# Kernel optimization log

Hardware: AMD Instinct MI355X
Metric: run time of the kernel (lower is better)

## Reference

```python
import jax, jax.numpy as jnp
import numpy as np

N_EMBD = 1024
N_HEAD = 16


def setup_inputs() -> dict:
    key = jax.random.key(0)
    ks = jax.random.split(key, 5)
    s = 0.02
    x = jax.random.normal(ks[0], (4, 2048, N_EMBD), dtype=jnp.float32)
    W_attn = jax.random.normal(ks[1], (N_EMBD, 3 * N_EMBD), dtype=jnp.float32) * s
    b_attn = jnp.zeros((3 * N_EMBD,), dtype=jnp.float32)
    W_proj = jax.random.normal(ks[2], (N_EMBD, N_EMBD), dtype=jnp.float32) * s
    b_proj = jnp.zeros((N_EMBD,), dtype=jnp.float32)
    return {"x": x, "W_attn": W_attn, "b_attn": b_attn, "W_proj": W_proj, "b_proj": b_proj}


def reference(x, W_attn, b_attn, W_proj, b_proj):
    B, T, C = x.shape
    H = N_HEAD
    D = C // H
    qkv = x @ W_attn + b_attn  # [B,T,3C]
    q, k, v = jnp.split(qkv, 3, axis=-1)
    # [B,H,T,D]
    q = q.reshape(B, T, H, D).transpose(0, 2, 1, 3)
    k = k.reshape(B, T, H, D).transpose(0, 2, 1, 3)
    v = v.reshape(B, T, H, D).transpose(0, 2, 1, 3)
    att = jnp.einsum('bhqd,bhkd->bhqk', q, k) * (1.0 / np.sqrt(D))
    causal = jnp.tril(jnp.ones((T, T), dtype=bool))
    att = jnp.where(causal[None, None], att, -jnp.inf)
    att = jax.nn.softmax(att, axis=-1)
    y = jnp.einsum('bhqk,bhkd->bhqd', att, v)
    y = y.transpose(0, 2, 1, 3).reshape(B, T, C)
    return y @ W_proj + b_proj
```

## Files before the change

kernel.cpp:

```cpp
#include <hip/hip_runtime.h>
#include <hip/hip_bf16.h>

#define B_ 4
#define T_ 2048
#define C_ 1024
#define H_ 16
#define D_ 64
#define N3_ 3072
#define M_ (B_*T_)

typedef __bf16 bf16x8 __attribute__((ext_vector_type(8)));
typedef float f32x4 __attribute__((ext_vector_type(4)));

__device__ __forceinline__ unsigned short f2bf(float f){
  __bf16 h = (__bf16)f;
  return __builtin_bit_cast(unsigned short, h);
}
__device__ __forceinline__ unsigned int pk2(float a, float b){
  return (unsigned int)f2bf(a) | ((unsigned int)f2bf(b)<<16);
}
__device__ __forceinline__ void gload_lds16(const unsigned short* g, unsigned short* l){
  __builtin_amdgcn_global_load_lds(
      (const __attribute__((address_space(1))) void*)g,
      (__attribute__((address_space(3))) void*)l, 16, 0, 0);
}

__global__ __launch_bounds__(256) void x_cvt(
    const float* __restrict__ X, unsigned short* __restrict__ Xb)
{
  const size_t i = ((size_t)blockIdx.x*256 + threadIdx.x)*8;
  float4 f0 = *(const float4*)(X+i);
  float4 f1 = *(const float4*)(X+i+4);
  uint4 w = make_uint4(pk2(f0.x,f0.y), pk2(f0.z,f0.w), pk2(f1.x,f1.y), pk2(f1.z,f1.w));
  *(uint4*)(Xb+i) = w;
}

__global__ __launch_bounds__(256) void transpose_cvt(
    const float* __restrict__ src, unsigned short* __restrict__ dst, int K, int N)
{
  __shared__ float tile[32][33];
  const int tx = threadIdx.x & 31, ty = threadIdx.x >> 5;
  const int nt = blockIdx.x * 32, kt = blockIdx.y * 32;
  #pragma unroll
  for (int i=0;i<32;i+=8) tile[ty+i][tx] = src[(size_t)(kt+ty+i)*N + nt+tx];
  __syncthreads();
  #pragma unroll
  for (int i=0;i<32;i+=8) dst[(size_t)(nt+ty+i)*K + kt+tx] = f2bf(tile[tx][ty+i]);
}

__global__ __launch_bounds__(256) void qkv_gemm(
    const unsigned short* __restrict__ Xb, const unsigned short* __restrict__ Wt,
    const float* __restrict__ bias,
    unsigned short* __restrict__ Qb, unsigned short* __restrict__ Kb,
    unsigned short* __restrict__ Vt)
{
  __shared__ __align__(16) unsigned short As[128][32];
  __shared__ __align__(16) unsigned short Bs[128][32];
  const int tid = threadIdx.x;
  const int nbx = N3_/128;
  const int cpx = (nbx*(M_/128))/8;
  const int id0 = (int)blockIdx.x;
  const int swz = (id0 & 7)*cpx + (id0 >> 3);
  const int m0 = (swz / nbx)*128, n0 = (swz % nbx)*128;
  const int wv = tid>>6, lane = tid&63, lm = lane&15, lq = lane>>4;
  const int wr = wv>>1, wc = wv&1;
  f32x4 acc[4][4] = {};
  const int schunk = (lane&3) ^ ((lane>>3)&3);
  const unsigned short* gA = Xb + (size_t)(m0 + wv*32 + (lane>>2))*C_ + schunk*8;
  const unsigned short* gB = Wt + (size_t)(n0 + wv*32 + (lane>>2))*C_ + schunk*8;
  unsigned short* lA0 = &As[wv*32][0];
  unsigned short* lA1 = &As[wv*32+16][0];
  unsigned short* lB0 = &Bs[wv*32][0];
  unsigned short* lB1 = &Bs[wv*32+16][0];
  const int rkey = (lm>>1)&3;
  for (int k0=0;k0<C_;k0+=32){
    __syncthreads();
    gload_lds16(gA + k0,            lA0);
    gload_lds16(gA + 16*C_ + k0,    lA1);
    gload_lds16(gB + k0,            lB0);
    gload_lds16(gB + 16*C_ + k0,    lB1);
    __syncthreads();
    bf16x8 a[4], b[4];
    #pragma unroll
    for (int mt=0;mt<4;mt++) a[mt] = *(const bf16x8*)&As[wr*64+mt*16+lm][(lq^rkey)*8];
    #pragma unroll
    for (int nt=0;nt<4;nt++) b[nt] = *(const bf16x8*)&Bs[wc*64+nt*16+lm][(lq^rkey)*8];
    #pragma unroll
    for (int mt=0;mt<4;mt++)
      #pragma unroll
      for (int nt=0;nt<4;nt++)
        acc[mt][nt] = __builtin_amdgcn_mfma_f32_16x16x32_bf16(a[mt], b[nt], acc[mt][nt], 0,0,0);
  }
  const int sel = n0>>10;
  const float qsc = (sel==0) ? 0.18033688f : 1.0f;
  #pragma unroll
  for (int mt=0;mt<4;mt++){
    const int grow = m0 + wr*64 + mt*16 + lq*4;
    const int bb = grow>>11, tt0 = grow&2047;
    #pragma unroll
    for (int nt=0;nt<4;nt++){
      const int gcol = n0 + wc*64 + nt*16 + lm;
      const int hh = (gcol>>6)&15, dd = gcol&63;
      const float bv = bias[gcol];
      if (sel==2){
        ushort4 pv;
        pv.x = f2bf(acc[mt][nt][0] + bv);
        pv.y = f2bf(acc[mt][nt][1] + bv);
        pv.z = f2bf(acc[mt][nt][2] + bv);
        pv.w = f2bf(acc[mt][nt][3] + bv);
        *(ushort4*)&Vt[ ((size_t)(bb*H_+hh)*D_ + dd)*T_ + tt0 ] = pv;
      } else {
        unsigned short* dst = (sel==0) ? Qb : Kb;
        #pragma unroll
        for (int r=0;r<4;r++)
          dst[ ((size_t)(bb*H_+hh)*T_ + tt0 + r)*D_ + dd ] = f2bf((acc[mt][nt][r] + bv)*qsc);
      }
    }
  }
}

__global__ __launch_bounds__(256, 4) void flash_attn(
    const unsigned short* __restrict__ Qb, const unsigned short* __restrict__ Kb,
    const unsigned short* __restrict__ Vt, unsigned short* __restrict__ Yb)
{
  __shared__ __align__(16) unsigned short Ks[2][64][64];
  __shared__ __align__(16) unsigned short Vs[2][64][64];
  __shared__ __align__(16) unsigned short Ps[64][64];
  const int tid = threadIdx.x;
  const int wv = tid>>6, lane = tid&63, lm = lane&15, lq = lane>>4;
  const int id = (int)blockIdx.x;
  const int bh = id & 63;
  const int qi = 31 - (id >> 6);
  const int qbase = qi*64;
  const unsigned short* Qh = Qb + (size_t)bh*T_*D_;
  const unsigned short* Kh = Kb + (size_t)bh*T_*D_;
  const unsigned short* Vh = Vt + (size_t)bh*D_*T_;
  bf16x8 aq[2];
  {
    const int q = qbase + wv*16 + lm;
    aq[0] = *(const bf16x8*)&Qh[(size_t)q*D_ + lq*8];
    aq[1] = *(const bf16x8*)&Qh[(size_t)q*D_ + 32 + lq*8];
  }
  f32x4 o[4] = {};
  float l_r[4] = {0.f,0.f,0.f,0.f};
  const int srl = lane>>3;
  const int sc  = (lane&7) ^ srl;
  const unsigned short* kg = Kh + (size_t)(wv*16 + srl)*D_ + sc*8;
  const unsigned short* vg = Vh + (size_t)(wv*16 + srl)*T_ + sc*8;
  const int keyR = lm&7;
  {
    unsigned short* lk = &Ks[0][wv*16][0];
    unsigned short* lv = &Vs[0][wv*16][0];
    gload_lds16(kg,            lk);
    gload_lds16(kg + 8*D_,     lk + 8*64);
    gload_lds16(vg,            lv);
    gload_lds16(vg + 8*T_,     lv + 8*64);
  }
  for (int j=0;j<=qi;j++){
    const int cb = j&1;
    __syncthreads();
    if (j < qi){
      unsigned short* lk = &Ks[cb^1][wv*16][0];
      unsigned short* lv = &Vs[cb^1][wv*16][0];
      gload_lds16(kg + (size_t)((j+1)*64  )*D_, lk);
      gload_lds16(kg + (size_t)((j+1)*64+8)*D_, lk + 8*64);
      gload_lds16(vg + (j+1)*64,                lv);
      gload_lds16(vg + 8*T_ + (j+1)*64,         lv + 8*64);
    }
    f32x4 s[4] = {};
    __builtin_amdgcn_s_setprio(1);
    #pragma unroll
    for (int nt=0;nt<4;nt++){
      bf16x8 bk0 = *(const bf16x8*)&Ks[cb][nt*16+lm][((lq  )^keyR)*8];
      bf16x8 bk1 = *(const bf16x8*)&Ks[cb][nt*16+lm][((lq+4)^keyR)*8];
      s[nt] = __builtin_amdgcn_mfma_f32_16x16x32_bf16(aq[0], bk0, s[nt], 0,0,0);
      s[nt] = __builtin_amdgcn_mfma_f32_16x16x32_bf16(aq[1], bk1, s[nt], 0,0,0);
    }
    __builtin_amdgcn_s_setprio(0);
    if (j==qi){
      const int qrow0 = wv*16 + lq*4;
      #pragma unroll
      for (int nt=0;nt<4;nt++){
        const int col = nt*16+lm;
        #pragma unroll
        for (int r=0;r<4;r++)
          s[nt][r] = (col <= qrow0+r) ? exp2f(s[nt][r]) : 0.f;
      }
    } else {
      #pragma unroll
      for (int nt=0;nt<4;nt++)
        #pragma unroll
        for (int r=0;r<4;r++)
          s[nt][r] = exp2f(s[nt][r]);
    }
    #pragma unroll
    for (int r=0;r<4;r++)
      l_r[r] += (s[0][r]+s[1][r]) + (s[2][r]+s[3][r]);
    #pragma unroll
    for (int nt=0;nt<4;nt++)
      #pragma unroll
      for (int r=0;r<4;r++){
        const int row = wv*16 + lq*4 + r;
        const int ch  = (2*nt + (lm>>3)) ^ (row&7);
        Ps[row][ch*8 + (lm&7)] = f2bf(s[nt][r]);
      }
    __builtin_amdgcn_s_setprio(1);
    #pragma unroll
    for (int kc=0;kc<2;kc++){
      bf16x8 ap = *(const bf16x8*)&Ps[wv*16+lm][((kc*4+lq)^keyR)*8];
      #pragma unroll
      for (int dt=0;dt<4;dt++){
        bf16x8 bv = *(const bf16x8*)&Vs[cb][dt*16+lm][((kc*4+lq)^keyR)*8];
        o[dt] = __builtin_amdgcn_mfma_f32_16x16x32_bf16(bv, ap, o[dt], 0,0,0);
      }
    }
    __builtin_amdgcn_s_setprio(0);
  }
  #pragma unroll
  for (int r=0;r<4;r++){
    float rs = l_r[r];
    rs += __shfl_xor(rs,1); rs += __shfl_xor(rs,2);
    rs += __shfl_xor(rs,4); rs += __shfl_xor(rs,8);
    l_r[r] = rs;
  }
  const int srcl = (lm>>2)<<4;
  float lv0v = __shfl(l_r[0], srcl);
  float lv1v = __shfl(l_r[1], srcl);
  float lv2v = __shfl(l_r[2], srcl);
  float lv3v = __shfl(l_r[3], srcl);
  const int rr = lm&3;
  float linv = (rr==0) ? lv0v : (rr==1) ? lv1v : (rr==2) ? lv2v : lv3v;
  linv = 1.0f/linv;
  const int bb = bh>>4, hh = bh&15;
  const int q = qbase + wv*16 + lm;
  #pragma unroll
  for (int dt=0;dt<4;dt++){
    ushort4 y;
    y.x = f2bf(o[dt][0]*linv);
    y.y = f2bf(o[dt][1]*linv);
    y.z = f2bf(o[dt][2]*linv);
    y.w = f2bf(o[dt][3]*linv);
    *(ushort4*)&Yb[ ((size_t)bb*T_ + q)*C_ + hh*64 + dt*16 + lq*4 ] = y;
  }
}

__global__ __launch_bounds__(256) void proj_gemm(
    const unsigned short* __restrict__ Yb, const unsigned short* __restrict__ Wt,
    const float* __restrict__ bias, float* __restrict__ Out)
{
  __shared__ __align__(16) unsigned short As[128][32];
  __shared__ __align__(16) unsigned short Bs[128][32];
  const int tid = threadIdx.x;
  const int nbx = C_/128;
  const int cpx = (nbx*(M_/128))/8;
  const int id0 = (int)blockIdx.x;
  const int swz = (id0 & 7)*cpx + (id0 >> 3);
  const int m0 = (swz / nbx)*128, n0 = (swz % nbx)*128;
  const int wv = tid>>6, lane = tid&63, lm = lane&15, lq = lane>>4;
  const int wr = wv>>1, wc = wv&1;
  f32x4 acc[4][4] = {};
  const int schunk = (lane&3) ^ ((lane>>3)&3);
  const unsigned short* gA = Yb + (size_t)(m0 + wv*32 + (lane>>2))*C_ + schunk*8;
  const unsigned short* gB = Wt + (size_t)(n0 + wv*32 + (lane>>2))*C_ + schunk*8;
  unsigned short* lA0 = &As[wv*32][0];
  unsigned short* lA1 = &As[wv*32+16][0];
  unsigned short* lB0 = &Bs[wv*32][0];
  unsigned short* lB1 = &Bs[wv*32+16][0];
  const int rkey = (lm>>1)&3;
  for (int k0=0;k0<C_;k0+=32){
    __syncthreads();
    gload_lds16(gA + k0,            lA0);
    gload_lds16(gA + 16*C_ + k0,    lA1);
    gload_lds16(gB + k0,            lB0);
    gload_lds16(gB + 16*C_ + k0,    lB1);
    __syncthreads();
    bf16x8 a[4], b[4];
    #pragma unroll
    for (int mt=0;mt<4;mt++) a[mt] = *(const bf16x8*)&As[wr*64+mt*16+lm][(lq^rkey)*8];
    #pragma unroll
    for (int nt=0;nt<4;nt++) b[nt] = *(const bf16x8*)&Bs[wc*64+nt*16+lm][(lq^rkey)*8];
    #pragma unroll
    for (int mt=0;mt<4;mt++)
      #pragma unroll
      for (int nt=0;nt<4;nt++)
        acc[mt][nt] = __builtin_amdgcn_mfma_f32_16x16x32_bf16(a[mt], b[nt], acc[mt][nt], 0,0,0);
  }
  #pragma unroll
  for (int mt=0;mt<4;mt++){
    const int grow = m0 + wr*64 + mt*16 + lq*4;
    #pragma unroll
    for (int nt=0;nt<4;nt++){
      const int gcol = n0 + wc*64 + nt*16 + lm;
      const float bv = bias[gcol];
      #pragma unroll
      for (int r=0;r<4;r++)
        Out[(size_t)(grow+r)*C_ + gcol] = acc[mt][nt][r] + bv;
    }
  }
}

extern "C" void kernel_launch(void* const* d_in, const int* in_sizes, int n_in,
                              void* d_out, int out_size, void* d_ws, size_t ws_size,
                              hipStream_t stream)
{
  const float* x      = (const float*)d_in[0];
  const float* W_attn = (const float*)d_in[1];
  const float* b_attn = (const float*)d_in[2];
  const float* W_proj = (const float*)d_in[3];
  const float* b_proj = (const float*)d_in[4];
  float* out = (float*)d_out;

  unsigned short* Wat = (unsigned short*)d_ws;
  unsigned short* Wpt = Wat + (size_t)N3_*C_;
  unsigned short* Xb  = Wpt + (size_t)C_*C_;
  unsigned short* Qb  = Xb  + (size_t)M_*C_;
  unsigned short* Kb  = Qb  + (size_t)M_*C_;
  unsigned short* Vt  = Kb  + (size_t)M_*C_;
  unsigned short* Yb  = Vt  + (size_t)M_*C_;
  (void)ws_size; (void)in_sizes; (void)n_in; (void)out_size;

  x_cvt        <<<dim3(M_*C_/2048),        256, 0, stream>>>(x, Xb);
  transpose_cvt<<<dim3(N3_/32, C_/32),     256, 0, stream>>>(W_attn, Wat, C_, N3_);
  transpose_cvt<<<dim3(C_/32,  C_/32),     256, 0, stream>>>(W_proj, Wpt, C_, C_);
  qkv_gemm     <<<dim3((N3_/128)*(M_/128)), 256, 0, stream>>>(Xb, Wat, b_attn, Qb, Kb, Vt);
  flash_attn   <<<dim3(2048),              256, 0, stream>>>(Qb, Kb, Vt, Yb);
  proj_gemm    <<<dim3((C_/128)*(M_/128)),  256, 0, stream>>>(Yb, Wpt, b_proj, out);
}
```

Before: 264.4 us.

## Restructure flash attention to 128-query blocks with 32x32 MFMA and register-resident P

The attention kernel now gives each block 128 queries (32 per wave) and uses 32x32x16 bf16 MFMAs, computing S transposed so P stays in registers. P is packed with v_cvt_pk_bf16_f32 and v_permlane32_swap instead of going through an LDS round trip. Each K/V tile loaded into LDS is now shared by twice as many queries, and the grid is halved. The costs are higher register pressure (occupancy hint lowered to 3), some waves idling on the diagonal tile, and coarser load balancing across blocks.

Result: faster. 251.2 us (-5.0%).

```diff
diff --git a/kernel.cpp b/kernel.cpp
--- a/kernel.cpp
+++ b/kernel.cpp
@@ -11,6 +11,7 @@
 
 typedef __bf16 bf16x8 __attribute__((ext_vector_type(8)));
 typedef float f32x4 __attribute__((ext_vector_type(4)));
+typedef float f32x16 __attribute__((ext_vector_type(16)));
 
 __device__ __forceinline__ unsigned short f2bf(float f){
   __bf16 h = (__bf16)f;
@@ -119,47 +120,68 @@
   }
 }
 
-__global__ __launch_bounds__(256, 4) void flash_attn(
+#define PV_CHUNK(SV, KG, C16) do{                                              \
+  unsigned int X0_, X1_, Y0_, Y1_;                                             \
+  asm("v_cvt_pk_bf16_f32 %0, %1, %2" : "=v"(X0_)                               \
+      : "v"((float)(SV)[(C16)*8+0]), "v"((float)(SV)[(C16)*8+1]));             \
+  asm("v_cvt_pk_bf16_f32 %0, %1, %2" : "=v"(X1_)                               \
+      : "v"((float)(SV)[(C16)*8+2]), "v"((float)(SV)[(C16)*8+3]));             \
+  asm("v_cvt_pk_bf16_f32 %0, %1, %2" : "=v"(Y0_)                               \
+      : "v"((float)(SV)[(C16)*8+4]), "v"((float)(SV)[(C16)*8+5]));             \
+  asm("v_cvt_pk_bf16_f32 %0, %1, %2" : "=v"(Y1_)                               \
+      : "v"((float)(SV)[(C16)*8+6]), "v"((float)(SV)[(C16)*8+7]));             \
+  asm volatile("v_permlane32_swap_b32 %0, %1" : "+v"(X0_), "+v"(Y0_));         \
+  asm volatile("v_permlane32_swap_b32 %0, %1" : "+v"(X1_), "+v"(Y1_));         \
+  uint4 pw_ = make_uint4(X0_, X1_, Y0_, Y1_);                                  \
+  bf16x8 pf_ = __builtin_bit_cast(bf16x8, pw_);                                \
+  const int ch_ = (((KG)*4 + (C16)*2 + hi) ^ l7)*8;                            \
+  bf16x8 v0_ = *(const bf16x8*)&Vs[cb][l31][ch_];                              \
+  bf16x8 v1_ = *(const bf16x8*)&Vs[cb][32+l31][ch_];                           \
+  o0 = __builtin_amdgcn_mfma_f32_32x32x16_bf16(v0_, pf_, o0, 0,0,0);           \
+  o1 = __builtin_amdgcn_mfma_f32_32x32x16_bf16(v1_, pf_, o1, 0,0,0);           \
+}while(0)
+
+__global__ __launch_bounds__(256, 3) void flash_attn(
     const unsigned short* __restrict__ Qb, const unsigned short* __restrict__ Kb,
     const unsigned short* __restrict__ Vt, unsigned short* __restrict__ Yb)
 {
   __shared__ __align__(16) unsigned short Ks[2][64][64];
   __shared__ __align__(16) unsigned short Vs[2][64][64];
-  __shared__ __align__(16) unsigned short Ps[64][64];
   const int tid = threadIdx.x;
-  const int wv = tid>>6, lane = tid&63, lm = lane&15, lq = lane>>4;
+  const int wv = tid>>6, lane = tid&63;
+  const int l31 = lane & 31, hi = lane >> 5, l7 = lane & 7;
   const int id = (int)blockIdx.x;
   const int bh = id & 63;
-  const int qi = 31 - (id >> 6);
-  const int qbase = qi*64;
+  const int qblk = 15 - (id >> 6);
+  const int qb = qblk*128;
+  const int q0 = qb + wv*32;
   const unsigned short* Qh = Qb + (size_t)bh*T_*D_;
   const unsigned short* Kh = Kb + (size_t)bh*T_*D_;
   const unsigned short* Vh = Vt + (size_t)bh*D_*T_;
-  bf16x8 aq[2];
-  {
-    const int q = qbase + wv*16 + lm;
-    aq[0] = *(const bf16x8*)&Qh[(size_t)q*D_ + lq*8];
-    aq[1] = *(const bf16x8*)&Qh[(size_t)q*D_ + 32 + lq*8];
-  }
-  f32x4 o[4] = {};
-  float l_r[4] = {0.f,0.f,0.f,0.f};
+  bf16x8 aq[4];
+  #pragma unroll
+  for (int kc=0;kc<4;kc++)
+    aq[kc] = *(const bf16x8*)&Qh[(size_t)(q0+l31)*D_ + kc*16 + hi*8];
+  f32x16 o0 = {}, o1 = {};
+  float l_r = 0.f;
   const int srl = lane>>3;
   const int sc  = (lane&7) ^ srl;
   const unsigned short* kg = Kh + (size_t)(wv*16 + srl)*D_ + sc*8;
   const unsigned short* vg = Vh + (size_t)(wv*16 + srl)*T_ + sc*8;
-  const int keyR = lm&7;
   {
     unsigned short* lk = &Ks[0][wv*16][0];
     unsigned short* lv = &Vs[0][wv*16][0];
-    gload_lds16(kg,            lk);
-    gload_lds16(kg + 8*D_,     lk + 8*64);
-    gload_lds16(vg,            lv);
-    gload_lds16(vg + 8*T_,     lv + 8*64);
-  }
-  for (int j=0;j<=qi;j++){
+    gload_lds16(kg,        lk);
+    gload_lds16(kg + 8*D_, lk + 8*64);
+    gload_lds16(vg,        lv);
+    gload_lds16(vg + 8*T_, lv + 8*64);
+  }
+  const int JT = 2*qblk + 2;
+  const int jmax = 2*qblk + (wv>>1);
+  for (int j=0;j<JT;j++){
     const int cb = j&1;
     __syncthreads();
-    if (j < qi){
+    if (j < JT-1){
       unsigned short* lk = &Ks[cb^1][wv*16][0];
       unsigned short* lv = &Vs[cb^1][wv*16][0];
       gload_lds16(kg + (size_t)((j+1)*64  )*D_, lk);
@@ -167,80 +189,53 @@
       gload_lds16(vg + (j+1)*64,                lv);
       gload_lds16(vg + 8*T_ + (j+1)*64,         lv + 8*64);
     }
-    f32x4 s[4] = {};
-    __builtin_amdgcn_s_setprio(1);
-    #pragma unroll
-    for (int nt=0;nt<4;nt++){
-      bf16x8 bk0 = *(const bf16x8*)&Ks[cb][nt*16+lm][((lq  )^keyR)*8];
-      bf16x8 bk1 = *(const bf16x8*)&Ks[cb][nt*16+lm][((lq+4)^keyR)*8];
-      s[nt] = __builtin_amdgcn_mfma_f32_16x16x32_bf16(aq[0], bk0, s[nt], 0,0,0);
-      s[nt] = __builtin_amdgcn_mfma_f32_16x16x32_bf16(aq[1], bk1, s[nt], 0,0,0);
+    if (j <= jmax){
+      f32x16 s0 = {}, s1 = {};
+      __builtin_amdgcn_s_setprio(1);
+      #pragma unroll
+      for (int kc=0;kc<4;kc++){
+        const int ch = ((kc*2+hi) ^ l7)*8;
+        bf16x8 k0 = *(const bf16x8*)&Ks[cb][l31][ch];
+        bf16x8 k1 = *(const bf16x8*)&Ks[cb][32+l31][ch];
+        s0 = __builtin_amdgcn_mfma_f32_32x32x16_bf16(k0, aq[kc], s0, 0,0,0);
+        s1 = __builtin_amdgcn_mfma_f32_32x32x16_bf16(k1, aq[kc], s1, 0,0,0);
+      }
+      __builtin_amdgcn_s_setprio(0);
+      if (j == jmax){
+        const int qrel = ((wv&1)<<5) + l31;
+        #pragma unroll
+        for (int r=0;r<16;r++){
+          const int koff = (r&3) + 8*(r>>2) + 4*hi;
+          s0[r] = (koff      <= qrel) ? exp2f(s0[r]) : 0.f;
+          s1[r] = (32 + koff <= qrel) ? exp2f(s1[r]) : 0.f;
+        }
+      } else {
+        #pragma unroll
+        for (int r=0;r<16;r++){ s0[r] = exp2f(s0[r]); s1[r] = exp2f(s1[r]); }
+      }
+      #pragma unroll
+      for (int r=0;r<16;r++) l_r += s0[r] + s1[r];
+      __builtin_amdgcn_s_setprio(1);
+      PV_CHUNK(s0, 0, 0); PV_CHUNK(s0, 0, 1);
+      PV_CHUNK(s1, 1, 0); PV_CHUNK(s1, 1, 1);
+      __builtin_amdgcn_s_setprio(0);
     }
-    __builtin_amdgcn_s_setprio(0);
-    if (j==qi){
-      const int qrow0 = wv*16 + lq*4;
-      #pragma unroll
-      for (int nt=0;nt<4;nt++){
-        const int col = nt*16+lm;
-        #pragma unroll
-        for (int r=0;r<4;r++)
-          s[nt][r] = (col <= qrow0+r) ? exp2f(s[nt][r]) : 0.f;
-      }
-    } else {
-      #pragma unroll
-      for (int nt=0;nt<4;nt++)
-        #pragma unroll
-        for (int r=0;r<4;r++)
-          s[nt][r] = exp2f(s[nt][r]);
-    }
-    #pragma unroll
-    for (int r=0;r<4;r++)
-      l_r[r] += (s[0][r]+s[1][r]) + (s[2][r]+s[3][r]);
-    #pragma unroll
-    for (int nt=0;nt<4;nt++)
-      #pragma unroll
-      for (int r=0;r<4;r++){
-        const int row = wv*16 + lq*4 + r;
-        const int ch  = (2*nt + (lm>>3)) ^ (row&7);
-        Ps[row][ch*8 + (lm&7)] = f2bf(s[nt][r]);
-      }
-    __builtin_amdgcn_s_setprio(1);
-    #pragma unroll
-    for (int kc=0;kc<2;kc++){
-      bf16x8 ap = *(const bf16x8*)&Ps[wv*16+lm][((kc*4+lq)^keyR)*8];
-      #pragma unroll
-      for (int dt=0;dt<4;dt++){
-        bf16x8 bv = *(const bf16x8*)&Vs[cb][dt*16+lm][((kc*4+lq)^keyR)*8];
-        o[dt] = __builtin_amdgcn_mfma_f32_16x16x32_bf16(bv, ap, o[dt], 0,0,0);
-      }
-    }
-    __builtin_amdgcn_s_setprio(0);
-  }
-  #pragma unroll
-  for (int r=0;r<4;r++){
-    float rs = l_r[r];
-    rs += __shfl_xor(rs,1); rs += __shfl_xor(rs,2);
-    rs += __shfl_xor(rs,4); rs += __shfl_xor(rs,8);
-    l_r[r] = rs;
-  }
-  const int srcl = (lm>>2)<<4;
-  float lv0v = __shfl(l_r[0], srcl);
-  float lv1v = __shfl(l_r[1], srcl);
-  float lv2v = __shfl(l_r[2], srcl);
-  float lv3v = __shfl(l_r[3], srcl);
-  const int rr = lm&3;
-  float linv = (rr==0) ? lv0v : (rr==1) ? lv1v : (rr==2) ? lv2v : lv3v;
-  linv = 1.0f/linv;
+  }
+  float rs = l_r + __shfl_xor(l_r, 32);
+  const float linv = 1.0f / rs;
   const int bb = bh>>4, hh = bh&15;
-  const int q = qbase + wv*16 + lm;
-  #pragma unroll
-  for (int dt=0;dt<4;dt++){
+  const int q = q0 + l31;
+  unsigned short* yrow = Yb + (size_t)(bb*T_ + q)*C_ + hh*64;
+  #pragma unroll
+  for (int g=0; g<4; g++){
     ushort4 y;
-    y.x = f2bf(o[dt][0]*linv);
-    y.y = f2bf(o[dt][1]*linv);
-    y.z = f2bf(o[dt][2]*linv);
-    y.w = f2bf(o[dt][3]*linv);
-    *(ushort4*)&Yb[ ((size_t)bb*T_ + q)*C_ + hh*64 + dt*16 + lq*4 ] = y;
+    y.x = f2bf(o0[4*g+0]*linv); y.y = f2bf(o0[4*g+1]*linv);
+    y.z = f2bf(o0[4*g+2]*linv); y.w = f2bf(o0[4*g+3]*linv);
+    *(ushort4*)&yrow[g*8 + hi*4] = y;
+    ushort4 z;
+    z.x = f2bf(o1[4*g+0]*linv); z.y = f2bf(o1[4*g+1]*linv);
+    z.z = f2bf(o1[4*g+2]*linv); z.w = f2bf(o1[4*g+3]*linv);
+    *(ushort4*)&yrow[32 + g*8 + hi*4] = z;
   }
 }
 
@@ -323,6 +318,6 @@
   transpose_cvt<<<dim3(N3_/32, C_/32),     256, 0, stream>>>(W_attn, Wat, C_, N3_);
   transpose_cvt<<<dim3(C_/32,  C_/32),     256, 0, stream>>>(W_proj, Wpt, C_, C_);
   qkv_gemm     <<<dim3((N3_/128)*(M_/128)), 256, 0, stream>>>(Xb, Wat, b_attn, Qb, Kb, Vt);
-  flash_attn   <<<dim3(2048),              256, 0, stream>>>(Qb, Kb, Vt, Yb);
+  flash_attn   <<<dim3(1024),              256, 0, stream>>>(Qb, Kb, Vt, Yb);
   proj_gemm    <<<dim3((C_/128)*(M_/128)),  256, 0, stream>>>(Yb, Wpt, b_proj, out);
 }
```
